# Performance work log

Measured on AMD Instinct MI355X. Metric: run time of the kernel, lower is better.

Reference implementation:

```python
import jax, jax.numpy as jnp
import numpy as np

B, S, IN_DIM = 8, 4096, 1024
N_SLOTS, SLOT_DIM, N_HEADS, CHUNK, TOP_K = 64, 256, 4, 16, 3
EPS_LN = 1e-5


def setup_inputs() -> dict:
    key = jax.random.key(0)
    ks = jax.random.split(key, 8)
    std = 0.02
    return {
        "x": jax.random.normal(ks[0], (B, S, IN_DIM), jnp.float32),
        "slot_memory": jax.random.normal(ks[1], (1, N_SLOTS, SLOT_DIM), jnp.float32) * std,
        "slot_keys": jax.random.normal(ks[2], (N_SLOTS, SLOT_DIM), jnp.float32) * std,
        "W_in": jax.random.normal(ks[3], (IN_DIM, SLOT_DIM), jnp.float32) / np.sqrt(IN_DIM).astype(np.float32),
        "W_write": jax.random.normal(ks[4], (SLOT_DIM, SLOT_DIM), jnp.float32) / np.sqrt(SLOT_DIM).astype(np.float32),
        "W_gate": jax.random.normal(ks[5], (2 * SLOT_DIM, 1), jnp.float32) / np.sqrt(2 * SLOT_DIM).astype(np.float32),
        "b_gate": jnp.zeros((1,), jnp.float32),
        "W_out": jax.random.normal(ks[6], (SLOT_DIM, IN_DIM), jnp.float32) / np.sqrt(SLOT_DIM).astype(np.float32),
        "ln_in_scale": jnp.ones((IN_DIM,), jnp.float32),
        "ln_in_bias": jnp.zeros((IN_DIM,), jnp.float32),
        "ln_s_scale": jnp.ones((SLOT_DIM,), jnp.float32),
        "ln_s_bias": jnp.zeros((SLOT_DIM,), jnp.float32),
    }


def _layer_norm(x, scale, bias):
    m = jnp.mean(x, axis=-1, keepdims=True)
    v = jnp.mean((x - m) ** 2, axis=-1, keepdims=True)
    return (x - m) * jax.lax.rsqrt(v + EPS_LN) * scale + bias


def _l2norm(x):
    n = jnp.sqrt(jnp.sum(x * x, axis=-1, keepdims=True))
    return x / jnp.maximum(n, 1e-12)  # matches F.normalize eps


def _forward(x, slot_memory, slot_keys, W_in, W_write, W_gate, b_gate, W_out,
             ln_in_scale, ln_in_bias, ln_s_scale, ln_s_bias):
    Bx, Sx, _ = x.shape
    hd = SLOT_DIM // N_HEADS
    slots0 = jnp.broadcast_to(slot_memory, (Bx, N_SLOTS, SLOT_DIM))

    # ---- batched read attention over slots ----
    q = _layer_norm(x, ln_in_scale, ln_in_bias) @ W_in          # (B,S,D)
    qh = q.reshape(Bx, Sx, N_HEADS, hd)
    kh = slots0.reshape(Bx, N_SLOTS, N_HEADS, hd)               # k == v == slots
    scores = jnp.einsum('bshd,bnhd->bhsn', qh, kh) * (hd ** -0.5)
    attn = jax.nn.softmax(scores, axis=-1)                      # (B,H,S,N)
    read = jnp.einsum('bhsn,bnhd->bshd', attn, kh).reshape(Bx, Sx, SLOT_DIM)

    # ---- sequential chunked top-k gather/scatter slot write ----
    key_norms = _l2norm(slot_keys)                              # (N,D)
    b_idx = jnp.arange(Bx)[:, None]

    def chunk_step(slots, chunk):                               # chunk: (B,C,D)
        summary = chunk.mean(axis=1)                            # (B,D)
        match = _l2norm(summary) @ key_norms.T                  # (B,N) cosine sim
        _, top_idx = jax.lax.top_k(match, TOP_K)                # (B,K)
        wv = summary @ W_write                                  # (B,D)
        sel = jnp.take_along_axis(slots, top_idx[:, :, None], axis=1)  # (B,K,D)
        gate = jax.nn.sigmoid(
            jnp.concatenate([sel.mean(axis=1), wv], axis=-1) @ W_gate + b_gate)  # (B,1)
        g = gate[:, None, :]
        new_vals = (1.0 - g) * sel + g * wv[:, None, :]         # (B,K,D)
        return slots.at[b_idx, top_idx].set(new_vals), None

    chunks = read.reshape(Bx, Sx // CHUNK, CHUNK, SLOT_DIM).transpose(1, 0, 2, 3)
    slots_f, _ = jax.lax.scan(chunk_step, slots0, chunks)
    new_slots = _layer_norm(slots_f, ln_s_scale, ln_s_bias)

    out = read @ W_out                                          # dropout is identity in eval
    return out, new_slots


def reference(x, slot_memory, slot_keys, W_in, W_write, W_gate, b_gate, W_out,
              ln_in_scale, ln_in_bias, ln_s_scale, ln_s_bias):
    return _forward(x, slot_memory, slot_keys, W_in, W_write, W_gate, b_gate, W_out,
                    ln_in_scale, ln_in_bias, ln_s_scale, ln_s_bias)
```

## Files before the change

### kernel.cpp

```cpp
#include <hip/hip_runtime.h>

typedef __attribute__((ext_vector_type(8))) short s8v;
typedef __attribute__((ext_vector_type(4))) float f4v;

#define PAD1 88

__device__ __forceinline__ unsigned short f2bf(float f) {
  unsigned u = __float_as_uint(f);
  u += 0x7fffu + ((u >> 16) & 1u);
  return (unsigned short)(u >> 16);
}
__device__ __forceinline__ float bf2f(unsigned short h) {
  return __uint_as_float(((unsigned)h) << 16);
}
__device__ __forceinline__ float rdlanef(float v, int l) {
  return __uint_as_float(__builtin_amdgcn_readlane(__float_as_uint(v), l));
}
__device__ __forceinline__ f4v vmax4(f4v a, f4v b) {
  f4v r; r[0]=fmaxf(a[0],b[0]); r[1]=fmaxf(a[1],b[1]); r[2]=fmaxf(a[2],b[2]); r[3]=fmaxf(a[3],b[3]); return r;
}
__device__ __forceinline__ f4v shflxor4(f4v v, int m) {
  f4v r; r[0]=__shfl_xor(v[0],m); r[1]=__shfl_xor(v[1],m); r[2]=__shfl_xor(v[2],m); r[3]=__shfl_xor(v[3],m); return r;
}
__device__ __forceinline__ f4v exp4(f4v v) {
  f4v r; r[0]=__expf(v[0]); r[1]=__expf(v[1]); r[2]=__expf(v[2]); r[3]=__expf(v[3]); return r;
}

__global__ void k_prep(const float* __restrict__ W_in, const float* __restrict__ lnis,
                       const float* __restrict__ lnib, const float* __restrict__ W_out,
                       const float* __restrict__ skeys, const float* __restrict__ smem0,
                       const float* __restrict__ wgate,
                       unsigned short* __restrict__ wth, unsigned short* __restrict__ wtl,
                       unsigned short* __restrict__ wot, float* __restrict__ keyn,
                       float* __restrict__ d0, float* __restrict__ uvec, float* __restrict__ vvec)
{
  __shared__ float pr[4];
  const int bid = blockIdx.x, tid = threadIdx.x;
  if (bid < 1024) {
    int idx = bid * 256 + tid;
    int n = idx >> 10, k = idx & 1023;
    float val = lnis[k] * W_in[k * 256 + n];
    unsigned short h = f2bf(val);
    wth[idx] = h;
    wtl[idx] = f2bf(val - bf2f(h));
  } else if (bid < 2048) {
    int idx = (bid - 1024) * 256 + tid;
    int n = idx >> 8, k = idx & 255;
    wot[idx] = f2bf(W_out[k * 1024 + n]);
  } else if (bid == 2048) {
    float su = 0.f, sv = 0.f;
    for (int i = 0; i < 1024; ++i) {
      float wv_ = W_in[i * 256 + tid];
      su += lnis[i] * wv_;
      sv += lnib[i] * wv_;
    }
    uvec[tid] = su; vvec[tid] = sv;
  } else {
    int n = bid - 2049;
    float sk = skeys[n * 256 + tid];
    float sq = sk * sk;
    #pragma unroll
    for (int m = 32; m; m >>= 1) sq += __shfl_xor(sq, m);
    if ((tid & 63) == 0) pr[tid >> 6] = sq;
    __syncthreads();
    float tot = pr[0] + pr[1] + pr[2] + pr[3];
    keyn[n * 256 + tid] = sk * (1.0f / fmaxf(sqrtf(tot), 1e-12f));
    float pd = smem0[n * 256 + tid] * wgate[tid];
    #pragma unroll
    for (int m = 32; m; m >>= 1) pd += __shfl_xor(pd, m);
    __syncthreads();
    if ((tid & 63) == 0) pr[tid >> 6] = pd;
    __syncthreads();
    if (tid == 0) d0[n] = pr[0] + pr[1] + pr[2] + pr[3];
  }
}

__global__ __launch_bounds__(512, 2) void k_gemm1(const float* __restrict__ x,
    const unsigned short* __restrict__ wth, const unsigned short* __restrict__ wtl,
    const float* __restrict__ uvec, const float* __restrict__ vvec,
    float* __restrict__ q)
{
  __shared__ unsigned short Ah[128 * PAD1], Al[128 * PAD1];
  __shared__ unsigned short Bh[256 * PAD1], Bl[256 * PAD1];
  __shared__ float uls[256], vls[256];
  __shared__ float mls[128], rls[128];
  const int tid = threadIdx.x;
  const int w = tid >> 6, lane = tid & 63;
  const int wm = w >> 2, wn = w & 3;
  const int row0 = blockIdx.x * 128;
  if (tid < 256) { uls[tid] = uvec[tid]; vls[tid] = vvec[tid]; }
  f4v zz = {0.f, 0.f, 0.f, 0.f};
  f4v acc[4][4];
  #pragma unroll
  for (int i = 0; i < 4; ++i)
    #pragma unroll
    for (int j = 0; j < 4; ++j) acc[i][j] = zz;
  const int rowA = tid >> 2, kqA = (tid & 3) * 16;
  const int colB = tid >> 1, khB = (tid & 1) * 32;
  float ps = 0.f, pss = 0.f;
  for (int kt = 0; kt < 16; ++kt) {
    const int k0 = kt * 64;
    {
      const float* src = x + (size_t)(row0 + rowA) * 1024 + k0 + kqA;
      float vv[16];
      #pragma unroll
      for (int i = 0; i < 4; ++i) *(f4v*)(vv + 4 * i) = *(const f4v*)(src + 4 * i);
      unsigned short hh[16], ll[16];
      #pragma unroll
      for (int i = 0; i < 16; ++i) {
        ps += vv[i]; pss += vv[i] * vv[i];
        unsigned short hsh = f2bf(vv[i]);
        hh[i] = hsh;
        ll[i] = f2bf(vv[i] - bf2f(hsh));
      }
      unsigned short* dh = &Ah[rowA * PAD1 + kqA];
      unsigned short* dl = &Al[rowA * PAD1 + kqA];
      *(s8v*)dh = *(const s8v*)hh; *(s8v*)(dh + 8) = *(const s8v*)(hh + 8);
      *(s8v*)dl = *(const s8v*)ll; *(s8v*)(dl + 8) = *(const s8v*)(ll + 8);
      const unsigned short* sh = wth + (size_t)colB * 1024 + k0 + khB;
      const unsigned short* sl = wtl + (size_t)colB * 1024 + k0 + khB;
      unsigned short* dbh = &Bh[colB * PAD1 + khB];
      unsigned short* dbl = &Bl[colB * PAD1 + khB];
      #pragma unroll
      for (int i = 0; i < 4; ++i) {
        *(s8v*)(dbh + 8 * i) = *(const s8v*)(sh + 8 * i);
        *(s8v*)(dbl + 8 * i) = *(const s8v*)(sl + 8 * i);
      }
    }
    __syncthreads();
    #pragma unroll
    for (int kk = 0; kk < 64; kk += 32) {
      const int kb = kk + (lane >> 4) * 8;
      s8v ah[4], al[4], bh[4], bl[4];
      #pragma unroll
      for (int mi = 0; mi < 4; ++mi) {
        const int rr = (wm * 64 + mi * 16 + (lane & 15)) * PAD1 + kb;
        ah[mi] = *(const s8v*)&Ah[rr];
        al[mi] = *(const s8v*)&Al[rr];
      }
      #pragma unroll
      for (int ni = 0; ni < 4; ++ni) {
        const int ccv = (wn * 64 + ni * 16 + (lane & 15)) * PAD1 + kb;
        bh[ni] = *(const s8v*)&Bh[ccv];
        bl[ni] = *(const s8v*)&Bl[ccv];
      }
      #pragma unroll
      for (int mi = 0; mi < 4; ++mi)
        #pragma unroll
        for (int ni = 0; ni < 4; ++ni) {
          acc[mi][ni] = __builtin_amdgcn_mfma_f32_16x16x32_bf16(ah[mi], bh[ni], acc[mi][ni], 0, 0, 0);
          acc[mi][ni] = __builtin_amdgcn_mfma_f32_16x16x32_bf16(ah[mi], bl[ni], acc[mi][ni], 0, 0, 0);
          acc[mi][ni] = __builtin_amdgcn_mfma_f32_16x16x32_bf16(al[mi], bh[ni], acc[mi][ni], 0, 0, 0);
        }
    }
    __syncthreads();
  }
  {
    float s0 = ps, s1 = pss;
    s0 += __shfl_xor(s0, 1); s1 += __shfl_xor(s1, 1);
    s0 += __shfl_xor(s0, 2); s1 += __shfl_xor(s1, 2);
    if ((tid & 3) == 0) {
      float mean = s0 * (1.0f / 1024.0f);
      mls[rowA] = mean;
      rls[rowA] = rsqrtf(s1 * (1.0f / 1024.0f) - mean * mean + 1e-5f);
    }
  }
  __syncthreads();
  #pragma unroll
  for (int mi = 0; mi < 4; ++mi)
    #pragma unroll
    for (int j = 0; j < 4; ++j) {
      const int lr = wm * 64 + mi * 16 + (lane >> 4) * 4 + j;
      const int r = row0 + lr;
      const float mv = mls[lr], rv = rls[lr];
      #pragma unroll
      for (int ni = 0; ni < 4; ++ni) {
        const int cidx = wn * 64 + ni * 16 + (lane & 15);
        q[(size_t)r * 256 + cidx] = rv * acc[mi][ni][j] - rv * mv * uls[cidx] + vls[cidx];
      }
    }
}

__global__ __launch_bounds__(512, 2) void k_attn(const float* __restrict__ q,
    const float* __restrict__ smem0, unsigned short* __restrict__ readb,
    float* __restrict__ summ)
{
  __shared__ float Kf[64 * 256];
  __shared__ float Pl[8][16 * 68];
  __shared__ float csm[8][64];
  const int tid = threadIdx.x;
  const int w = tid >> 6, lane = tid & 63;
  const int h = w & 3;
  const int l15 = lane & 15, kq = lane >> 4;

  {
    const int base = tid * 32;
    #pragma unroll
    for (int i = 0; i < 8; ++i)
      *(f4v*)&Kf[base + i * 4] = *(const f4v*)&smem0[base + i * 4];
  }
  __syncthreads();

  s8v bsh[4][2], bsl[4][2], bpv[4][2];
  #pragma unroll
  for (int nt = 0; nt < 4; ++nt)
    #pragma unroll
    for (int ks = 0; ks < 2; ++ks) {
      const float* src = &Kf[(nt * 16 + l15) * 256 + h * 64 + ks * 32 + kq * 8];
      float tmp[8];
      *(f4v*)tmp = *(const f4v*)src; *(f4v*)(tmp + 4) = *(const f4v*)(src + 4);
      unsigned short hh[8], ll[8];
      #pragma unroll
      for (int j = 0; j < 8; ++j) {
        hh[j] = f2bf(tmp[j]);
        ll[j] = f2bf(tmp[j] - bf2f(hh[j]));
      }
      bsh[nt][ks] = *(const s8v*)hh;
      bsl[nt][ks] = *(const s8v*)ll;
      unsigned short pp[8];
      #pragma unroll
      for (int j = 0; j < 8; ++j)
        pp[j] = f2bf(Kf[(ks * 32 + kq * 8 + j) * 256 + h * 64 + nt * 16 + l15]);
      bpv[nt][ks] = *(const s8v*)pp;
    }

  const int g0 = blockIdx.x * 8 + (w >> 2) * 4;
  f4v qv[2][4];
  {
    #pragma unroll
    for (int ks = 0; ks < 2; ++ks) {
      const float* qp = q + (size_t)(g0 * 16 + l15) * 256 + h * 64 + ks * 32 + kq * 8;
      qv[0][ks * 2] = *(const f4v*)qp;
      qv[0][ks * 2 + 1] = *(const f4v*)(qp + 4);
    }
  }
  #pragma unroll
  for (int i = 0; i < 4; ++i) {
    const int cur = i & 1, nxt = cur ^ 1;
    if (i < 3) {
      const int gn = g0 + i + 1;
      #pragma unroll
      for (int ks = 0; ks < 2; ++ks) {
        const float* qp = q + (size_t)(gn * 16 + l15) * 256 + h * 64 + ks * 32 + kq * 8;
        qv[nxt][ks * 2] = *(const f4v*)qp;
        qv[nxt][ks * 2 + 1] = *(const f4v*)(qp + 4);
      }
    }
    const int g = g0 + i;
    s8v ah[2], al[2];
    #pragma unroll
    for (int ks = 0; ks < 2; ++ks) {
      float tmp[8];
      *(f4v*)tmp = qv[cur][ks * 2]; *(f4v*)(tmp + 4) = qv[cur][ks * 2 + 1];
      unsigned short hh[8], ll[8];
      #pragma unroll
      for (int j = 0; j < 8; ++j) {
        hh[j] = f2bf(tmp[j]);
        ll[j] = f2bf(tmp[j] - bf2f(hh[j]));
      }
      ah[ks] = *(const s8v*)hh; al[ks] = *(const s8v*)ll;
    }
    f4v zz = {0.f, 0.f, 0.f, 0.f};
    f4v sacc[4] = {zz, zz, zz, zz};
    #pragma unroll
    for (int ks = 0; ks < 2; ++ks)
      #pragma unroll
      for (int nt = 0; nt < 4; ++nt) {
        sacc[nt] = __builtin_amdgcn_mfma_f32_16x16x32_bf16(ah[ks], bsh[nt][ks], sacc[nt], 0, 0, 0);
        sacc[nt] = __builtin_amdgcn_mfma_f32_16x16x32_bf16(ah[ks], bsl[nt][ks], sacc[nt], 0, 0, 0);
        sacc[nt] = __builtin_amdgcn_mfma_f32_16x16x32_bf16(al[ks], bsh[nt][ks], sacc[nt], 0, 0, 0);
      }
    #pragma unroll
    for (int nt = 0; nt < 4; ++nt) sacc[nt] = sacc[nt] * 0.125f;
    f4v mx = vmax4(vmax4(sacc[0], sacc[1]), vmax4(sacc[2], sacc[3]));
    #pragma unroll
    for (int m = 1; m <= 8; m <<= 1) mx = vmax4(mx, shflxor4(mx, m));
    f4v p[4];
    f4v psum = zz;
    #pragma unroll
    for (int nt = 0; nt < 4; ++nt) { p[nt] = exp4(sacc[nt] - mx); psum = psum + p[nt]; }
    #pragma unroll
    for (int m = 1; m <= 8; m <<= 1) psum = psum + shflxor4(psum, m);
    f4v rs;
    rs[0] = 1.0f / psum[0]; rs[1] = 1.0f / psum[1];
    rs[2] = 1.0f / psum[2]; rs[3] = 1.0f / psum[3];
    #pragma unroll
    for (int nt = 0; nt < 4; ++nt) p[nt] = p[nt] * rs;
    float cs4[4];
    #pragma unroll
    for (int nt = 0; nt < 4; ++nt) {
      cs4[nt] = p[nt][0] + p[nt][1] + p[nt][2] + p[nt][3];
      cs4[nt] += __shfl_xor(cs4[nt], 16);
      cs4[nt] += __shfl_xor(cs4[nt], 32);
    }
    if (kq == 0) {
      #pragma unroll
      for (int nt = 0; nt < 4; ++nt) csm[w][nt * 16 + l15] = cs4[nt];
    }
    #pragma unroll
    for (int nt = 0; nt < 4; ++nt)
      #pragma unroll
      for (int j = 0; j < 4; ++j)
        Pl[w][(kq * 4 + j) * 68 + nt * 16 + l15] = p[nt][j];
    s8v pa[2];
    #pragma unroll
    for (int ks = 0; ks < 2; ++ks) {
      const float* pp = &Pl[w][l15 * 68 + ks * 32 + kq * 8];
      float tmp[8];
      *(f4v*)tmp = *(const f4v*)pp; *(f4v*)(tmp + 4) = *(const f4v*)(pp + 4);
      unsigned short uu[8];
      #pragma unroll
      for (int j = 0; j < 8; ++j) uu[j] = f2bf(tmp[j]);
      pa[ks] = *(const s8v*)uu;
    }
    f4v racc[4] = {zz, zz, zz, zz};
    #pragma unroll
    for (int ks = 0; ks < 2; ++ks)
      #pragma unroll
      for (int nt = 0; nt < 4; ++nt)
        racc[nt] = __builtin_amdgcn_mfma_f32_16x16x32_bf16(pa[ks], bpv[nt][ks], racc[nt], 0, 0, 0);
    const int rowbase = (g >> 8) * 4096 + (g & 255) * 16;
    #pragma unroll
    for (int nt = 0; nt < 4; ++nt)
      #pragma unroll
      for (int j = 0; j < 4; ++j)
        readb[(size_t)(rowbase + kq * 4 + j) * 256 + h * 64 + nt * 16 + l15] = f2bf(racc[nt][j]);
    float s = 0.f;
    #pragma unroll 8
    for (int n = 0; n < 64; ++n) s += csm[w][n] * Kf[n * 256 + h * 64 + lane];
    summ[(size_t)g * 256 + h * 64 + lane] = s * (1.0f / 16.0f);
  }
}

__global__ void k_match(const float* __restrict__ summ, const float* __restrict__ keyn,
                        const float* __restrict__ Wwr, const float* __restrict__ wgate,
                        int* __restrict__ top3, float* __restrict__ wv,
                        float* __restrict__ wg2, float* __restrict__ dwv)
{
  __shared__ float sm[4][256];
  __shared__ float nrm_inv[4];
  __shared__ float mtch[4][64];
  __shared__ float redA[4][4], redB[4][4];
  const int tid = threadIdx.x, lane = tid & 63, w = tid >> 6;
  const int gbase = blockIdx.x * 4;
  #pragma unroll
  for (int gi = 0; gi < 4; ++gi) sm[gi][tid] = summ[(size_t)(gbase + gi) * 256 + tid];
  __syncthreads();
  {
    float ss = 0.f;
    #pragma unroll
    for (int i = 0; i < 4; ++i) { float vv_ = sm[w][lane + i * 64]; ss += vv_ * vv_; }
    #pragma unroll
    for (int m = 32; m; m >>= 1) ss += __shfl_xor(ss, m);
    if (lane == 0) nrm_inv[w] = 1.0f / fmaxf(sqrtf(ss), 1e-12f);
  }
  __syncthreads();
  {
    const int n = tid >> 2, qq = tid & 3;
    float mac[4] = {0.f, 0.f, 0.f, 0.f};
    const float* kp = keyn + n * 256 + qq * 64;
    for (int d = 0; d < 64; ++d) {
      float kv = kp[d];
      int dd = qq * 64 + d;
      mac[0] += sm[0][dd] * kv; mac[1] += sm[1][dd] * kv;
      mac[2] += sm[2][dd] * kv; mac[3] += sm[3][dd] * kv;
    }
    #pragma unroll
    for (int gi = 0; gi < 4; ++gi) {
      float v2_ = mac[gi];
      v2_ += __shfl_xor(v2_, 1);
      v2_ += __shfl_xor(v2_, 2);
      if (qq == 0) mtch[gi][n] = v2_ * nrm_inv[gi];
    }
  }
  __syncthreads();
  {
    float vorig = mtch[w][lane];
    #pragma unroll
    for (int it = 0; it < 3; ++it) {
      float rv = vorig; int ri = lane;
      #pragma unroll
      for (int m = 32; m; m >>= 1) {
        float ov = __shfl_xor(rv, m); int oi = __shfl_xor(ri, m);
        if (ov > rv || (ov == rv && oi < ri)) { rv = ov; ri = oi; }
      }
      if (lane == 0) top3[(gbase + w) * 4 + it] = ri;
      if (lane == ri) vorig = -3.0e38f;
    }
  }
  float wva[4] = {0.f, 0.f, 0.f, 0.f};
  for (int d = 0; d < 256; ++d) {
    float ww = Wwr[(size_t)d * 256 + tid];
    wva[0] += sm[0][d] * ww; wva[1] += sm[1][d] * ww;
    wva[2] += sm[2][d] * ww; wva[3] += sm[3][d] * ww;
  }
  const float g1 = wgate[tid], g2 = wgate[256 + tid];
  #pragma unroll
  for (int gi = 0; gi < 4; ++gi) {
    wv[(size_t)(gbase + gi) * 256 + tid] = wva[gi];
    float p2 = wva[gi] * g2, p1 = wva[gi] * g1;
    #pragma unroll
    for (int m = 32; m; m >>= 1) { p2 += __shfl_xor(p2, m); p1 += __shfl_xor(p1, m); }
    if (lane == 0) { redA[gi][w] = p2; redB[gi][w] = p1; }
  }
  __syncthreads();
  if (tid < 4) {
    wg2[gbase + tid] = redA[tid][0] + redA[tid][1] + redA[tid][2] + redA[tid][3];
    dwv[gbase + tid] = redB[tid][0] + redB[tid][1] + redB[tid][2] + redB[tid][3];
  }
}

__global__ __launch_bounds__(1024) void k_scan(const float* __restrict__ d0,
    const int* __restrict__ top3, const float* __restrict__ wg2, const float* __restrict__ dwv,
    const float* __restrict__ bgate, const float* __restrict__ wv,
    const float* __restrict__ smem0, const float* __restrict__ lnss,
    const float* __restrict__ lnsb, float* __restrict__ outns)
{
  __shared__ float Wl[256][64];
  __shared__ float pn[64];
  __shared__ float wvs[32][256];
  const int bb = blockIdx.x, tid = threadIdx.x;

  if (tid < 64) {
    const int lane = tid;
    const float bg = bgate[0];
    const float L2E = 1.4426950408889634f;
    const float COEFN = -0.48089834696298783f;
    int ixA[4], iyA[4], izA[4];
    float wzA[4], dvA[4], goA[4];
    #pragma unroll
    for (int j = 0; j < 4; ++j) {
      const int c = j * 64 + lane;
      int4 t3 = *(const int4*)&top3[(bb * 256 + c) * 4];
      ixA[j] = t3.x; iyA[j] = t3.y; izA[j] = t3.z;
      wzA[j] = -(wg2[bb * 256 + c] + bg) * L2E;
      dvA[j] = dwv[bb * 256 + c];
      goA[j] = 0.f;
    }
    float dn = d0[lane];
    int i0p = 255, i1p = 255, i2p = 255;
    float gp = 0.f, dvp = 0.f;
    int i0c = __builtin_amdgcn_readlane(ixA[0], 0);
    int i1c = __builtin_amdgcn_readlane(iyA[0], 0);
    int i2c = __builtin_amdgcn_readlane(izA[0], 0);
    float wzc = rdlanef(wzA[0], 0), dvc = rdlanef(dvA[0], 0);
    float P0 = rdlanef(dn, i0c), P1 = rdlanef(dn, i1c), P2 = rdlanef(dn, i2c);

    auto step = [&](int sl, int nix, int niy, int niz, float nwz, float ndv,
                    int nsl, bool dopull, float& goref) {
      float m0 = (i0c == i0p || i0c == i1p || i0c == i2p) ? gp : 0.f;
      float m1 = (i1c == i0p || i1c == i1p || i1c == i2p) ? gp : 0.f;
      float m2 = (i2c == i0p || i2c == i1p || i2c == i2p) ? gp : 0.f;
      P0 = fmaf(m0, dvp - P0, P0);
      P1 = fmaf(m1, dvp - P1, P1);
      P2 = fmaf(m2, dvp - P2, P2);
      float s3 = P0 + P1 + P2;
      float e = __builtin_amdgcn_exp2f(fmaf(s3, COEFN, wzc));
      float g = __builtin_amdgcn_rcpf(1.0f + e);
      goref = (lane == sl) ? g : goref;
      bool hit = (lane == i0p) | (lane == i1p) | (lane == i2p);
      float ml = hit ? gp : 0.f;
      dn = fmaf(ml, dvp - dn, dn);
      i0p = i0c; i1p = i1c; i2p = i2c; gp = g; dvp = dvc;
      if (dopull) {
        i0c = __builtin_amdgcn_readlane(nix, nsl);
        i1c = __builtin_amdgcn_readlane(niy, nsl);
        i2c = __builtin_amdgcn_readlane(niz, nsl);
        wzc = rdlanef(nwz, nsl); dvc = rdlanef(ndv, nsl);
        P0 = rdlanef(dn, i0c); P1 = rdlanef(dn, i1c); P2 = rdlanef(dn, i2c);
      }
    };

    #pragma unroll
    for (int j = 0; j < 4; ++j) {
      #pragma unroll 1
      for (int sl = 0; sl < 63; ++sl)
        step(sl, ixA[j], iyA[j], izA[j], wzA[j], dvA[j], sl + 1, true, goA[j]);
      if (j < 3)
        step(63, ixA[j + 1], iyA[j + 1], izA[j + 1], wzA[j + 1], dvA[j + 1], 0, true, goA[j]);
      else
        step(63, ixA[3], iyA[3], izA[3], wzA[3], dvA[3], 0, false, goA[j]);
    }

    float running = 1.0f;
    #pragma unroll
    for (int j = 3; j >= 0; --j) {
      #pragma unroll 1
      for (int sl = 63; sl >= 0; --sl) {
        const int a0 = __builtin_amdgcn_readlane(ixA[j], sl);
        const int a1 = __builtin_amdgcn_readlane(iyA[j], sl);
        const int a2 = __builtin_amdgcn_readlane(izA[j], sl);
        const float gv = rdlanef(goA[j], sl);
        const bool hit = (lane == a0) | (lane == a1) | (lane == a2);
        Wl[j * 64 + sl][lane] = hit ? gv * running : 0.f;
        running = hit ? running * (1.0f - gv) : running;
      }
    }
    pn[lane] = running;
  }
  __syncthreads();

  const int n = tid >> 4, dq = tid & 15;
  float acc[16];
  {
    const float p = pn[n];
    const float* v0p = smem0 + n * 256 + dq * 16;
    #pragma unroll
    for (int i = 0; i < 16; i += 4) {
      f4v v0 = *(const f4v*)(v0p + i);
      acc[i] = p * v0[0]; acc[i + 1] = p * v0[1];
      acc[i + 2] = p * v0[2]; acc[i + 3] = p * v0[3];
    }
  }
  const int rr = tid >> 5, cc8 = (tid & 31) * 8;
  for (int ct = 0; ct < 8; ++ct) {
    __syncthreads();
    {
      const float* src = wv + (size_t)(bb * 256 + ct * 32 + rr) * 256 + cc8;
      *(f4v*)&wvs[rr][cc8] = *(const f4v*)src;
      *(f4v*)&wvs[rr][cc8 + 4] = *(const f4v*)(src + 4);
    }
    __syncthreads();
    #pragma unroll 1
    for (int cc = 0; cc < 32; ++cc) {
      const float coef = Wl[ct * 32 + cc][n];
      if (coef != 0.f) {
        const float* wp = &wvs[cc][dq * 16];
        #pragma unroll
        for (int i4 = 0; i4 < 4; ++i4) {
          f4v wq = *(const f4v*)(wp + i4 * 4);
          acc[i4 * 4 + 0] += coef * wq[0];
          acc[i4 * 4 + 1] += coef * wq[1];
          acc[i4 * 4 + 2] += coef * wq[2];
          acc[i4 * 4 + 3] += coef * wq[3];
        }
      }
    }
  }

  float s1 = 0.f;
  #pragma unroll
  for (int i = 0; i < 16; ++i) s1 += acc[i];
  #pragma unroll
  for (int m = 1; m < 16; m <<= 1) s1 += __shfl_xor(s1, m);
  const float mean = s1 * (1.0f / 256.0f);
  float s2 = 0.f;
  #pragma unroll
  for (int i = 0; i < 16; ++i) { float dd = acc[i] - mean; s2 += dd * dd; }
  #pragma unroll
  for (int m = 1; m < 16; m <<= 1) s2 += __shfl_xor(s2, m);
  const float rstd = rsqrtf(s2 * (1.0f / 256.0f) + 1e-5f);
  {
    const int base = (bb * 64 + n) * 256 + dq * 16;
    #pragma unroll
    for (int i = 0; i < 16; ++i) {
      int dd = dq * 16 + i;
      outns[base + i] = (acc[i] - mean) * rstd * lnss[dd] + lnsb[dd];
    }
  }
}

__global__ __launch_bounds__(512, 2) void k_gemm2(const unsigned short* __restrict__ a,
    const unsigned short* __restrict__ wot, float* __restrict__ out)
{
  __shared__ unsigned short As[128 * PAD1];
  __shared__ unsigned short Bs[256 * PAD1];
  const int tid = threadIdx.x;
  const int w = tid >> 6, lane = tid & 63;
  const int wm = w >> 2, wn = w & 3;
  const int mblk = blockIdx.x >> 2, nblk = blockIdx.x & 3;
  const int row0 = mblk * 128, n0 = nblk * 256;
  f4v zz = {0.f, 0.f, 0.f, 0.f};
  f4v acc[4][4];
  #pragma unroll
  for (int i = 0; i < 4; ++i)
    #pragma unroll
    for (int j = 0; j < 4; ++j) acc[i][j] = zz;
  const int rowA = tid >> 2, kqA = (tid & 3) * 16;
  const int colB = tid >> 1, khB = (tid & 1) * 32;
  for (int kt = 0; kt < 4; ++kt) {
    const int k0 = kt * 64;
    {
      const unsigned short* src = a + (size_t)(row0 + rowA) * 256 + k0 + kqA;
      *(s8v*)&As[rowA * PAD1 + kqA] = *(const s8v*)src;
      *(s8v*)&As[rowA * PAD1 + kqA + 8] = *(const s8v*)(src + 8);
      const unsigned short* sb = wot + (size_t)(n0 + colB) * 256 + k0 + khB;
      unsigned short* db = &Bs[colB * PAD1 + khB];
      #pragma unroll
      for (int i = 0; i < 4; ++i) *(s8v*)(db + 8 * i) = *(const s8v*)(sb + 8 * i);
    }
    __syncthreads();
    #pragma unroll
    for (int kk = 0; kk < 64; kk += 32) {
      const int kb = kk + (lane >> 4) * 8;
      s8v af[4], bf[4];
      #pragma unroll
      for (int mi = 0; mi < 4; ++mi)
        af[mi] = *(const s8v*)&As[(wm * 64 + mi * 16 + (lane & 15)) * PAD1 + kb];
      #pragma unroll
      for (int ni = 0; ni < 4; ++ni)
        bf[ni] = *(const s8v*)&Bs[(wn * 64 + ni * 16 + (lane & 15)) * PAD1 + kb];
      #pragma unroll
      for (int mi = 0; mi < 4; ++mi)
        #pragma unroll
        for (int ni = 0; ni < 4; ++ni)
          acc[mi][ni] = __builtin_amdgcn_mfma_f32_16x16x32_bf16(af[mi], bf[ni], acc[mi][ni], 0, 0, 0);
    }
    __syncthreads();
  }
  #pragma unroll
  for (int mi = 0; mi < 4; ++mi)
    #pragma unroll
    for (int j = 0; j < 4; ++j) {
      const int r = row0 + wm * 64 + mi * 16 + (lane >> 4) * 4 + j;
      #pragma unroll
      for (int ni = 0; ni < 4; ++ni) {
        const int cidx = wn * 64 + ni * 16 + (lane & 15);
        out[(size_t)r * 1024 + n0 + cidx] = acc[mi][ni][j];
      }
    }
}

extern "C" void kernel_launch(void* const* d_in, const int* in_sizes, int n_in,
                              void* d_out, int out_size, void* d_ws, size_t ws_size,
                              hipStream_t stream) {
  const float* x      = (const float*)d_in[0];
  const float* smem   = (const float*)d_in[1];
  const float* skeys  = (const float*)d_in[2];
  const float* W_in   = (const float*)d_in[3];
  const float* W_wr   = (const float*)d_in[4];
  const float* wgate  = (const float*)d_in[5];
  const float* bgate  = (const float*)d_in[6];
  const float* W_out  = (const float*)d_in[7];
  const float* lnis   = (const float*)d_in[8];
  const float* lnib   = (const float*)d_in[9];
  const float* lnss   = (const float*)d_in[10];
  const float* lnsb   = (const float*)d_in[11];
  (void)in_sizes; (void)n_in; (void)out_size; (void)ws_size;

  char* ws = (char*)d_ws;
  float*          q_buf = (float*)(ws + 0);
  unsigned short* readb = (unsigned short*)(ws + 134217728);
  float*          summ  = (float*)(ws + 150994944);
  float*          wv    = (float*)(ws + 153092096);
  unsigned short* wth   = (unsigned short*)(ws + 155189248);
  unsigned short* wtl   = (unsigned short*)(ws + 155713536);
  unsigned short* wot   = (unsigned short*)(ws + 156237824);
  float*          keyn  = (float*)(ws + 156762112);
  float*          uvec  = (float*)(ws + 157089792);
  float*          vvec  = (float*)(ws + 157090816);
  float*          d0    = (float*)(ws + 157091840);
  int*            top3  = (int*)(ws + 157092096);
  float*          wg2   = (float*)(ws + 157124864);
  float*          dwv   = (float*)(ws + 157133056);

  float* out   = (float*)d_out;
  float* outns = out + 33554432;

  k_prep<<<dim3(2113), dim3(256), 0, stream>>>(W_in, lnis, lnib, W_out, skeys, smem, wgate,
                                               wth, wtl, wot, keyn, d0, uvec, vvec);
  k_gemm1<<<dim3(256), dim3(512), 0, stream>>>(x, wth, wtl, uvec, vvec, q_buf);
  k_attn<<<dim3(256), dim3(512), 0, stream>>>(q_buf, smem, readb, summ);
  k_match<<<dim3(512), dim3(256), 0, stream>>>(summ, keyn, W_wr, wgate, top3, wv, wg2, dwv);
  k_scan<<<dim3(8), dim3(1024), 0, stream>>>(d0, top3, wg2, dwv, bgate, wv, smem, lnss, lnsb, outns);
  k_gemm2<<<dim3(1024), dim3(512), 0, stream>>>(readb, wot, out);
}
```

Before: 364.4 us.

## Shrink GEMM1 K-tile to 32 and serialize scan gate recurrence in LDS

The first GEMM's K tile drops from 64 to 32, with a tighter LDS padding and twice as many iterations. This cuts shared memory per block, likely to fit more resident blocks, at the cost of more barriers. The scan kernel's sequential gate recurrence no longer uses a wavefront-wide readlane pipeline. A single thread now walks the 256 steps, reading and updating the 64 slot dot-products in LDS with packed indices, which trades cross-lane bookkeeping for a scalar dependency chain through LDS.

```diff
diff --git a/kernel.cpp b/kernel.cpp
--- a/kernel.cpp
+++ b/kernel.cpp
@@ -4,6 +4,7 @@
 typedef __attribute__((ext_vector_type(4))) float f4v;
 
 #define PAD1 88
+#define PADK 40
 
 __device__ __forceinline__ unsigned short f2bf(float f) {
   unsigned u = __float_as_uint(f);
@@ -12,9 +13,6 @@
 }
 __device__ __forceinline__ float bf2f(unsigned short h) {
   return __uint_as_float(((unsigned)h) << 16);
-}
-__device__ __forceinline__ float rdlanef(float v, int l) {
-  return __uint_as_float(__builtin_amdgcn_readlane(__float_as_uint(v), l));
 }
 __device__ __forceinline__ f4v vmax4(f4v a, f4v b) {
   f4v r; r[0]=fmaxf(a[0],b[0]); r[1]=fmaxf(a[1],b[1]); r[2]=fmaxf(a[2],b[2]); r[3]=fmaxf(a[3],b[3]); return r;
@@ -80,8 +78,8 @@
     const float* __restrict__ uvec, const float* __restrict__ vvec,
     float* __restrict__ q)
 {
-  __shared__ unsigned short Ah[128 * PAD1], Al[128 * PAD1];
-  __shared__ unsigned short Bh[256 * PAD1], Bl[256 * PAD1];
+  __shared__ unsigned short Ah[128 * PADK], Al[128 * PADK];
+  __shared__ unsigned short Bh[256 * PADK], Bl[256 * PADK];
   __shared__ float uls[256], vls[256];
   __shared__ float mls[128], rls[128];
   const int tid = threadIdx.x;
@@ -95,52 +93,46 @@
   for (int i = 0; i < 4; ++i)
     #pragma unroll
     for (int j = 0; j < 4; ++j) acc[i][j] = zz;
-  const int rowA = tid >> 2, kqA = (tid & 3) * 16;
-  const int colB = tid >> 1, khB = (tid & 1) * 32;
+  const int rowA = tid >> 2, kqA = (tid & 3) * 8;
+  const int colB = tid >> 1, khB = (tid & 1) * 16;
   float ps = 0.f, pss = 0.f;
-  for (int kt = 0; kt < 16; ++kt) {
-    const int k0 = kt * 64;
+  for (int kt = 0; kt < 32; ++kt) {
+    const int k0 = kt * 32;
     {
       const float* src = x + (size_t)(row0 + rowA) * 1024 + k0 + kqA;
-      float vv[16];
-      #pragma unroll
-      for (int i = 0; i < 4; ++i) *(f4v*)(vv + 4 * i) = *(const f4v*)(src + 4 * i);
-      unsigned short hh[16], ll[16];
-      #pragma unroll
-      for (int i = 0; i < 16; ++i) {
+      float vv[8];
+      *(f4v*)vv = *(const f4v*)src;
+      *(f4v*)(vv + 4) = *(const f4v*)(src + 4);
+      unsigned short hh[8], ll[8];
+      #pragma unroll
+      for (int i = 0; i < 8; ++i) {
         ps += vv[i]; pss += vv[i] * vv[i];
         unsigned short hsh = f2bf(vv[i]);
         hh[i] = hsh;
         ll[i] = f2bf(vv[i] - bf2f(hsh));
       }
-      unsigned short* dh = &Ah[rowA * PAD1 + kqA];
-      unsigned short* dl = &Al[rowA * PAD1 + kqA];
-      *(s8v*)dh = *(const s8v*)hh; *(s8v*)(dh + 8) = *(const s8v*)(hh + 8);
-      *(s8v*)dl = *(const s8v*)ll; *(s8v*)(dl + 8) = *(const s8v*)(ll + 8);
+      *(s8v*)&Ah[rowA * PADK + kqA] = *(const s8v*)hh;
+      *(s8v*)&Al[rowA * PADK + kqA] = *(const s8v*)ll;
       const unsigned short* sh = wth + (size_t)colB * 1024 + k0 + khB;
       const unsigned short* sl = wtl + (size_t)colB * 1024 + k0 + khB;
-      unsigned short* dbh = &Bh[colB * PAD1 + khB];
-      unsigned short* dbl = &Bl[colB * PAD1 + khB];
-      #pragma unroll
-      for (int i = 0; i < 4; ++i) {
-        *(s8v*)(dbh + 8 * i) = *(const s8v*)(sh + 8 * i);
-        *(s8v*)(dbl + 8 * i) = *(const s8v*)(sl + 8 * i);
-      }
-    }
-    __syncthreads();
-    #pragma unroll
-    for (int kk = 0; kk < 64; kk += 32) {
-      const int kb = kk + (lane >> 4) * 8;
+      *(s8v*)&Bh[colB * PADK + khB] = *(const s8v*)sh;
+      *(s8v*)&Bh[colB * PADK + khB + 8] = *(const s8v*)(sh + 8);
+      *(s8v*)&Bl[colB * PADK + khB] = *(const s8v*)sl;
+      *(s8v*)&Bl[colB * PADK + khB + 8] = *(const s8v*)(sl + 8);
+    }
+    __syncthreads();
+    {
+      const int kb = (lane >> 4) * 8;
       s8v ah[4], al[4], bh[4], bl[4];
       #pragma unroll
       for (int mi = 0; mi < 4; ++mi) {
-        const int rr = (wm * 64 + mi * 16 + (lane & 15)) * PAD1 + kb;
+        const int rr = (wm * 64 + mi * 16 + (lane & 15)) * PADK + kb;
         ah[mi] = *(const s8v*)&Ah[rr];
         al[mi] = *(const s8v*)&Al[rr];
       }
       #pragma unroll
       for (int ni = 0; ni < 4; ++ni) {
-        const int ccv = (wn * 64 + ni * 16 + (lane & 15)) * PAD1 + kb;
+        const int ccv = (wn * 64 + ni * 16 + (lane & 15)) * PADK + kb;
         bh[ni] = *(const s8v*)&Bh[ccv];
         bl[ni] = *(const s8v*)&Bl[ccv];
       }
@@ -419,69 +411,51 @@
   __shared__ float Wl[256][64];
   __shared__ float pn[64];
   __shared__ float wvs[32][256];
+  __shared__ float gls[256];
+  __shared__ int   pprm[256][4];
+  __shared__ float dsl[64];
   const int bb = blockIdx.x, tid = threadIdx.x;
-
+  const int lane = tid & 63;
+
+  int ixA[4], iyA[4], izA[4];
   if (tid < 64) {
-    const int lane = tid;
     const float bg = bgate[0];
     const float L2E = 1.4426950408889634f;
-    const float COEFN = -0.48089834696298783f;
-    int ixA[4], iyA[4], izA[4];
-    float wzA[4], dvA[4], goA[4];
     #pragma unroll
     for (int j = 0; j < 4; ++j) {
-      const int c = j * 64 + lane;
+      const int c = j * 64 + tid;
       int4 t3 = *(const int4*)&top3[(bb * 256 + c) * 4];
       ixA[j] = t3.x; iyA[j] = t3.y; izA[j] = t3.z;
-      wzA[j] = -(wg2[bb * 256 + c] + bg) * L2E;
-      dvA[j] = dwv[bb * 256 + c];
-      goA[j] = 0.f;
-    }
-    float dn = d0[lane];
-    int i0p = 255, i1p = 255, i2p = 255;
-    float gp = 0.f, dvp = 0.f;
-    int i0c = __builtin_amdgcn_readlane(ixA[0], 0);
-    int i1c = __builtin_amdgcn_readlane(iyA[0], 0);
-    int i2c = __builtin_amdgcn_readlane(izA[0], 0);
-    float wzc = rdlanef(wzA[0], 0), dvc = rdlanef(dvA[0], 0);
-    float P0 = rdlanef(dn, i0c), P1 = rdlanef(dn, i1c), P2 = rdlanef(dn, i2c);
-
-    auto step = [&](int sl, int nix, int niy, int niz, float nwz, float ndv,
-                    int nsl, bool dopull, float& goref) {
-      float m0 = (i0c == i0p || i0c == i1p || i0c == i2p) ? gp : 0.f;
-      float m1 = (i1c == i0p || i1c == i1p || i1c == i2p) ? gp : 0.f;
-      float m2 = (i2c == i0p || i2c == i1p || i2c == i2p) ? gp : 0.f;
-      P0 = fmaf(m0, dvp - P0, P0);
-      P1 = fmaf(m1, dvp - P1, P1);
-      P2 = fmaf(m2, dvp - P2, P2);
-      float s3 = P0 + P1 + P2;
-      float e = __builtin_amdgcn_exp2f(fmaf(s3, COEFN, wzc));
-      float g = __builtin_amdgcn_rcpf(1.0f + e);
-      goref = (lane == sl) ? g : goref;
-      bool hit = (lane == i0p) | (lane == i1p) | (lane == i2p);
-      float ml = hit ? gp : 0.f;
-      dn = fmaf(ml, dvp - dn, dn);
-      i0p = i0c; i1p = i1c; i2p = i2c; gp = g; dvp = dvc;
-      if (dopull) {
-        i0c = __builtin_amdgcn_readlane(nix, nsl);
-        i1c = __builtin_amdgcn_readlane(niy, nsl);
-        i2c = __builtin_amdgcn_readlane(niz, nsl);
-        wzc = rdlanef(nwz, nsl); dvc = rdlanef(ndv, nsl);
-        P0 = rdlanef(dn, i0c); P1 = rdlanef(dn, i1c); P2 = rdlanef(dn, i2c);
-      }
-    };
-
-    #pragma unroll
-    for (int j = 0; j < 4; ++j) {
-      #pragma unroll 1
-      for (int sl = 0; sl < 63; ++sl)
-        step(sl, ixA[j], iyA[j], izA[j], wzA[j], dvA[j], sl + 1, true, goA[j]);
-      if (j < 3)
-        step(63, ixA[j + 1], iyA[j + 1], izA[j + 1], wzA[j + 1], dvA[j + 1], 0, true, goA[j]);
-      else
-        step(63, ixA[3], iyA[3], izA[3], wzA[3], dvA[3], 0, false, goA[j]);
-    }
-
+      pprm[c][0] = t3.x | (t3.y << 6) | (t3.z << 12);
+      pprm[c][1] = __float_as_int(-(wg2[bb * 256 + c] + bg) * L2E);
+      pprm[c][2] = __float_as_int(dwv[bb * 256 + c]);
+      pprm[c][3] = 0;
+    }
+    dsl[tid] = d0[tid];
+  }
+  __syncthreads();
+
+  if (tid == 0) {
+    const float COEFN = -0.48089834696298783f;
+    #pragma unroll 2
+    for (int c = 0; c < 256; ++c) {
+      const int4 pr = *(const int4*)&pprm[c][0];
+      const int i0 = pr.x & 63, i1 = (pr.x >> 6) & 63, i2 = (pr.x >> 12) & 63;
+      const float wz = __int_as_float(pr.y);
+      const float dv = __int_as_float(pr.z);
+      const float a = dsl[i0], b = dsl[i1], d2 = dsl[i2];
+      const float s3 = a + b + d2;
+      const float e = __builtin_amdgcn_exp2f(fmaf(s3, COEFN, wz));
+      const float g = __builtin_amdgcn_rcpf(1.0f + e);
+      gls[c] = g;
+      dsl[i0] = fmaf(g, dv - a, a);
+      dsl[i1] = fmaf(g, dv - b, b);
+      dsl[i2] = fmaf(g, dv - d2, d2);
+    }
+  }
+  __syncthreads();
+
+  if (tid < 64) {
     float running = 1.0f;
     #pragma unroll
     for (int j = 3; j >= 0; --j) {
@@ -490,7 +464,7 @@
         const int a0 = __builtin_amdgcn_readlane(ixA[j], sl);
         const int a1 = __builtin_amdgcn_readlane(iyA[j], sl);
         const int a2 = __builtin_amdgcn_readlane(izA[j], sl);
-        const float gv = rdlanef(goA[j], sl);
+        const float gv = gls[j * 64 + sl];
         const bool hit = (lane == a0) | (lane == a1) | (lane == a2);
         Wl[j * 64 + sl][lane] = hit ? gv * running : 0.f;
         running = hit ? running * (1.0f - gv) : running;
```

Result: faster. 354.4 us (-2.8%).
